# Optimization experiments

Measured on AMD Instinct MI355X. Metric: run time of the kernel, lower is better.

The kernel has to match this reference:

```python
import jax, jax.numpy as jnp
import numpy as np
import math

B, S, E, H = 2, 2048, 1024, 16
D = E // H  # head_dim = 64


def setup_inputs() -> dict:
    key = jax.random.key(0)
    ks = jax.random.split(key, 5)
    scale_p = 1.0 / math.sqrt(D)
    return {
        "x": jax.random.normal(ks[0], (B, S, E), dtype=jnp.float32),
        "Wq": jax.random.normal(ks[1], (D, D), dtype=jnp.float32) * scale_p,
        "Wk": jax.random.normal(ks[2], (D, D), dtype=jnp.float32) * scale_p,
        "Wv": jax.random.normal(ks[3], (D, D), dtype=jnp.float32) * scale_p,
        "W_out": jax.random.normal(ks[4], (E, E), dtype=jnp.float32) * (1.0 / math.sqrt(E)),
        "b_out": jnp.zeros((E,), dtype=jnp.float32),
    }


def reference(x, Wq, Wk, Wv, W_out, b_out):
    b, s, e = x.shape
    xh = x.reshape(b, s, H, D)  # [B,S,H,D]
    # per-head linear projections (torch Linear: y = x @ W.T), weights shared across heads
    q = jnp.einsum("bshd,ed->bshe", xh, Wq)
    k = jnp.einsum("bshd,ed->bshe", xh, Wk)
    v = jnp.einsum("bshd,ed->bshe", xh, Wv)
    # scaled dot-product attention, scale = sqrt(embed_dim) per tutorial-style impl
    energy = jnp.einsum("bqhd,bkhd->bhqk", q, k) / jnp.sqrt(jnp.float32(e))
    attn = jax.nn.softmax(energy, axis=-1)  # [B,H,S,S]
    out = jnp.einsum("bhqk,bkhd->bqhd", attn, v).reshape(b, s, e)
    return out @ W_out.T + b_out
```

## Files before the change

### kernel.cpp

```cpp
#include <hip/hip_runtime.h>
#include <math.h>

#define BB 2
#define SS 2048
#define EE 1024
#define HH 16
#define DD 64
constexpr int NROWS = BB * SS * HH;
constexpr float SCALE_Q = 1.4426950408889634f / 32.0f;

typedef __attribute__((ext_vector_type(8))) short bf16x8;
typedef __attribute__((ext_vector_type(4))) float f32x4;
typedef __attribute__((ext_vector_type(16))) float f32x16;
typedef __attribute__((ext_vector_type(4))) unsigned u32x4;

__device__ inline ushort f2bf(float f) {
  unsigned u = __builtin_bit_cast(unsigned, f);
  u += 0x7fffu + ((u >> 16) & 1u);
  return (ushort)(u >> 16);
}

__device__ inline unsigned cvt_pk(float lo, float hi) {
  unsigned r;
  asm("v_cvt_pk_bf16_f32 %0, %1, %2" : "=v"(r) : "v"(lo), "v"(hi));
  return r;
}

__global__ __launch_bounds__(256) void wconv(
    const float* __restrict__ Wq, const float* __restrict__ Wk,
    const float* __restrict__ Wv, const float* __restrict__ Wo,
    ushort* __restrict__ wqkvb, ushort* __restrict__ wob) {
  int idx = blockIdx.x * 256 + threadIdx.x;
  const float* sp;
  ushort* dp;
  if (idx < 1536) {
    int t = idx >> 9, j = idx & 511;
    const float* W = (t == 0) ? Wq : ((t == 1) ? Wk : Wv);
    sp = W + j * 8;
    dp = wqkvb + t * 4096 + j * 8;
  } else {
    size_t j = (size_t)(idx - 1536) * 8;
    sp = Wo + j;
    dp = wob + j;
  }
  float4 a = *(const float4*)sp;
  float4 c = *(const float4*)(sp + 4);
  u32x4 r;
  r[0] = cvt_pk(a.x, a.y);
  r[1] = cvt_pk(a.z, a.w);
  r[2] = cvt_pk(c.x, c.y);
  r[3] = cvt_pk(c.z, c.w);
  *(u32x4*)dp = r;
}

__global__ __launch_bounds__(256) void qkv_mfma(
    const float* __restrict__ x, const ushort* __restrict__ wqkv,
    ushort* __restrict__ qo, ushort* __restrict__ ko, ushort* __restrict__ vto) {
  __shared__ __align__(16) ushort Xs[128 * 72];
  __shared__ __align__(16) ushort Ws[3][64 * 72];
  const int tid = threadIdx.x, w = tid >> 6, l = tid & 63;
  const int g = l >> 4, c = l & 15;
  const int s0 = blockIdx.x * 128, h = blockIdx.y, b = blockIdx.z;

  for (int i = tid; i < 1536; i += 256) {
    int t = i >> 9, j = i & 511;
    int r = j >> 3, e0 = (j & 7) * 8;
    *(bf16x8*)&Ws[t][r * 72 + e0] = *(const bf16x8*)&wqkv[t * 4096 + r * 64 + e0];
  }
  for (int i = tid; i < 2048; i += 256) {
    int r = i >> 4, c4 = (i & 15) * 4;
    float4 xv = *(const float4*)&x[(((size_t)b * SS + s0 + r) * HH + h) * DD + c4];
    uint2 pk;
    pk.x = cvt_pk(xv.x, xv.y);
    pk.y = cvt_pk(xv.z, xv.w);
    *(uint2*)&Xs[r * 72 + c4] = pk;
  }
  __syncthreads();

  bf16x8 a_[2][2];
#pragma unroll
  for (int rf = 0; rf < 2; ++rf) {
    a_[rf][0] = *(bf16x8*)&Xs[(w * 32 + rf * 16 + c) * 72 + g * 8];
    a_[rf][1] = *(bf16x8*)&Xs[(w * 32 + rf * 16 + c) * 72 + 32 + g * 8];
  }

#pragma unroll
  for (int t = 0; t < 2; ++t) {
    ushort* out = (t == 0) ? qo : ko;
    const float sc = (t == 0) ? SCALE_Q : 1.0f;
#pragma unroll
    for (int ct = 0; ct < 4; ++ct) {
      bf16x8 b0 = *(bf16x8*)&Ws[t][(ct * 16 + c) * 72 + g * 8];
      bf16x8 b1 = *(bf16x8*)&Ws[t][(ct * 16 + c) * 72 + 32 + g * 8];
#pragma unroll
      for (int rf = 0; rf < 2; ++rf) {
        f32x4 acc = (f32x4){0.f, 0.f, 0.f, 0.f};
        acc = __builtin_amdgcn_mfma_f32_16x16x32_bf16(a_[rf][0], b0, acc, 0, 0, 0);
        acc = __builtin_amdgcn_mfma_f32_16x16x32_bf16(a_[rf][1], b1, acc, 0, 0, 0);
#pragma unroll
        for (int r = 0; r < 4; ++r) {
          int srow = w * 32 + rf * 16 + g * 4 + r;
          out[(((size_t)b * SS + s0 + srow) * HH + h) * DD + ct * 16 + c] =
              f2bf(acc[r] * sc);
        }
      }
    }
  }
#pragma unroll
  for (int ct = 0; ct < 4; ++ct) {
    bf16x8 b0 = *(bf16x8*)&Ws[2][(ct * 16 + c) * 72 + g * 8];
    bf16x8 b1 = *(bf16x8*)&Ws[2][(ct * 16 + c) * 72 + 32 + g * 8];
#pragma unroll
    for (int rf = 0; rf < 2; ++rf) {
      f32x4 acc = (f32x4){0.f, 0.f, 0.f, 0.f};
      acc = __builtin_amdgcn_mfma_f32_16x16x32_bf16(a_[rf][0], b0, acc, 0, 0, 0);
      acc = __builtin_amdgcn_mfma_f32_16x16x32_bf16(a_[rf][1], b1, acc, 0, 0, 0);
      uint2 pk;
      pk.x = cvt_pk(acc[0], acc[1]);
      pk.y = cvt_pk(acc[2], acc[3]);
      int d = ct * 16 + c;
      int srow = w * 32 + rf * 16 + g * 4;
      *(uint2*)&vto[(((size_t)b * HH + h) * DD + d) * SS + s0 + srow] = pk;
    }
  }
}

__global__ __launch_bounds__(256, 1) void attn_mfma(
    const ushort* __restrict__ q, const ushort* __restrict__ k,
    const ushort* __restrict__ vt, ushort* __restrict__ o) {
  __shared__ __align__(16) ushort Ks[2][64 * 72];
  __shared__ __align__(16) ushort Vts[2][64 * 72];
  const int tid = threadIdx.x, w = tid >> 6, l = tid & 63;
  const int lq = l & 31, h2 = l >> 5;
  const int work = ((blockIdx.x & 7) << 5) | (blockIdx.x >> 3);
  const int qt = work & 7, hb = work >> 3;
  const int h = hb & 15, b = hb >> 4;
  const int q0 = qt * 256 + w * 64;

  const size_t bh_qk = (size_t)b * SS * EE + h * DD;
  const size_t bh_vt = (size_t)b * SS * EE + h * (DD * SS);

  const int sr0 = tid >> 3;
  const int se0 = (tid & 7) * 8;
  const int krow0 = (sr0 & 19) | ((sr0 & 4) << 1) | ((sr0 & 8) >> 1);

  {
    bf16x8 kr0 = *(const bf16x8*)&k[bh_qk + (size_t)sr0 * EE + se0];
    bf16x8 kr1 = *(const bf16x8*)&k[bh_qk + (size_t)(sr0 + 32) * EE + se0];
    bf16x8 vr0 = *(const bf16x8*)&vt[bh_vt + (size_t)sr0 * SS + se0];
    bf16x8 vr1 = *(const bf16x8*)&vt[bh_vt + (size_t)(sr0 + 32) * SS + se0];
    *(bf16x8*)&Ks[0][krow0 * 72 + se0] = kr0;
    *(bf16x8*)&Ks[0][(krow0 + 32) * 72 + se0] = kr1;
    *(bf16x8*)&Vts[0][sr0 * 72 + se0] = vr0;
    *(bf16x8*)&Vts[0][(sr0 + 32) * 72 + se0] = vr1;
  }

  bf16x8 aq[2][4];
#pragma unroll
  for (int qb = 0; qb < 2; ++qb)
#pragma unroll
    for (int db = 0; db < 4; ++db)
      aq[qb][db] = *(const bf16x8*)&q[bh_qk +
          (size_t)(q0 + qb * 32 + lq) * EE + db * 16 + h2 * 8];

  f32x16 accO[2][2];
  float lacc[2][2];
#pragma unroll
  for (int qb = 0; qb < 2; ++qb) {
    lacc[qb][0] = 0.f;
    lacc[qb][1] = 0.f;
#pragma unroll
    for (int ct = 0; ct < 2; ++ct)
#pragma unroll
      for (int r = 0; r < 16; ++r) accO[qb][ct][r] = 0.f;
  }

  __syncthreads();

  for (int t = 0; t < 32; ++t) {
    const int cur = t & 1;
    bf16x8 kr0, kr1, vr0, vr1;
    if (t < 31) {
      const size_t kb2 = bh_qk + (size_t)((t + 1) * 64) * EE;
      kr0 = *(const bf16x8*)&k[kb2 + (size_t)sr0 * EE + se0];
      kr1 = *(const bf16x8*)&k[kb2 + (size_t)(sr0 + 32) * EE + se0];
      const size_t vb2 = bh_vt + (t + 1) * 64;
      vr0 = *(const bf16x8*)&vt[vb2 + (size_t)sr0 * SS + se0];
      vr1 = *(const bf16x8*)&vt[vb2 + (size_t)(sr0 + 32) * SS + se0];
    }

    bf16x8 kf[2][4];
#pragma unroll
    for (int kb = 0; kb < 2; ++kb)
#pragma unroll
      for (int db = 0; db < 4; ++db)
        kf[kb][db] = *(bf16x8*)&Ks[cur][(kb * 32 + lq) * 72 + db * 16 + h2 * 8];

    u32x4 pwv[2][2][2];
#pragma unroll
    for (int qb = 0; qb < 2; ++qb) {
      f32x16 s[2];
      __builtin_amdgcn_s_setprio(1);
#pragma unroll
      for (int kb = 0; kb < 2; ++kb) {
        f32x16 acc;
#pragma unroll
        for (int r = 0; r < 16; ++r) acc[r] = 0.f;
#pragma unroll
        for (int db = 0; db < 4; ++db)
          acc = __builtin_amdgcn_mfma_f32_32x32x16_bf16(kf[kb][db], aq[qb][db],
                                                        acc, 0, 0, 0);
        s[kb] = acc;
      }
      __builtin_amdgcn_s_setprio(0);
#pragma unroll
      for (int kb = 0; kb < 2; ++kb)
#pragma unroll
        for (int t16 = 0; t16 < 2; ++t16)
#pragma unroll
          for (int j2 = 0; j2 < 4; ++j2) {
            float pa = __builtin_amdgcn_exp2f(s[kb][t16 * 8 + j2 * 2]);
            float pb = __builtin_amdgcn_exp2f(s[kb][t16 * 8 + j2 * 2 + 1]);
            lacc[qb][kb] += pa + pb;
            pwv[qb][kb][t16][j2] = cvt_pk(pa, pb);
          }
    }

    bf16x8 vf[2][4];
#pragma unroll
    for (int ct = 0; ct < 2; ++ct)
#pragma unroll
      for (int kb = 0; kb < 2; ++kb)
#pragma unroll
        for (int t16 = 0; t16 < 2; ++t16)
          vf[ct][kb * 2 + t16] = *(bf16x8*)&Vts[cur][(ct * 32 + lq) * 72 +
                                                     kb * 32 + t16 * 16 + h2 * 8];

    __builtin_amdgcn_s_setprio(1);
#pragma unroll
    for (int ct = 0; ct < 2; ++ct)
#pragma unroll
      for (int kb = 0; kb < 2; ++kb)
#pragma unroll
        for (int t16 = 0; t16 < 2; ++t16) {
          accO[0][ct] = __builtin_amdgcn_mfma_f32_32x32x16_bf16(
              vf[ct][kb * 2 + t16],
              __builtin_bit_cast(bf16x8, pwv[0][kb][t16]), accO[0][ct], 0, 0, 0);
          accO[1][ct] = __builtin_amdgcn_mfma_f32_32x32x16_bf16(
              vf[ct][kb * 2 + t16],
              __builtin_bit_cast(bf16x8, pwv[1][kb][t16]), accO[1][ct], 0, 0, 0);
        }
    __builtin_amdgcn_s_setprio(0);

    if (t < 31) {
      const int nxt = cur ^ 1;
      *(bf16x8*)&Ks[nxt][krow0 * 72 + se0] = kr0;
      *(bf16x8*)&Ks[nxt][(krow0 + 32) * 72 + se0] = kr1;
      *(bf16x8*)&Vts[nxt][sr0 * 72 + se0] = vr0;
      *(bf16x8*)&Vts[nxt][(sr0 + 32) * 72 + se0] = vr1;
    }
    __syncthreads();
  }

#pragma unroll
  for (int qb = 0; qb < 2; ++qb) {
    float tsum = lacc[qb][0] + lacc[qb][1];
    tsum += __shfl_xor(tsum, 32, 64);
    float inv = 1.f / tsum;
    size_t row = (size_t)b * SS + q0 + qb * 32 + lq;
#pragma unroll
    for (int ct = 0; ct < 2; ++ct)
#pragma unroll
      for (int rq = 0; rq < 4; ++rq) {
        uint2 pk;
        pk.x = cvt_pk(accO[qb][ct][rq * 4 + 0] * inv,
                      accO[qb][ct][rq * 4 + 1] * inv);
        pk.y = cvt_pk(accO[qb][ct][rq * 4 + 2] * inv,
                      accO[qb][ct][rq * 4 + 3] * inv);
        *(uint2*)&o[row * EE + h * DD + ct * 32 + rq * 8 + h2 * 4] = pk;
      }
  }
}

__global__ __launch_bounds__(256) void out_proj_mfma(
    const ushort* __restrict__ a, const ushort* __restrict__ wo,
    const float* __restrict__ bias, float* __restrict__ y) {
  __shared__ __align__(16) ushort As[2][128 * 72];
  __shared__ __align__(16) ushort Ws[2][64 * 72];
  const int tid = threadIdx.x, w = tid >> 6, l = tid & 63;
  const int g = l >> 4, c = l & 15;
  const int m0 = blockIdx.x * 128, n0 = blockIdx.y * 64;
  const int sr = tid >> 3, se = (tid & 7) * 8;

  f32x4 acc[2][4];
#pragma unroll
  for (int mf = 0; mf < 2; ++mf)
#pragma unroll
    for (int ct = 0; ct < 4; ++ct) acc[mf][ct] = (f32x4){0.f, 0.f, 0.f, 0.f};

  {
#pragma unroll
    for (int j = 0; j < 4; ++j) {
      int r = sr + j * 32;
      *(bf16x8*)&As[0][r * 72 + se] = *(const bf16x8*)&a[(size_t)(m0 + r) * EE + se];
    }
#pragma unroll
    for (int j = 0; j < 2; ++j) {
      int r = sr + j * 32;
      *(bf16x8*)&Ws[0][r * 72 + se] = *(const bf16x8*)&wo[(size_t)(n0 + r) * EE + se];
    }
  }
  __syncthreads();

  for (int t = 0; t < 16; ++t) {
    const int cur = t & 1;
    bf16x8 Arg[4], Brg[2];
    if (t < 15) {
      const int k0 = (t + 1) * 64;
#pragma unroll
      for (int j = 0; j < 4; ++j) {
        int r = sr + j * 32;
        Arg[j] = *(const bf16x8*)&a[(size_t)(m0 + r) * EE + k0 + se];
      }
#pragma unroll
      for (int j = 0; j < 2; ++j) {
        int r = sr + j * 32;
        Brg[j] = *(const bf16x8*)&wo[(size_t)(n0 + r) * EE + k0 + se];
      }
    }

    bf16x8 af[2][2];
#pragma unroll
    for (int mf = 0; mf < 2; ++mf) {
      af[mf][0] = *(bf16x8*)&As[cur][(w * 32 + mf * 16 + c) * 72 + g * 8];
      af[mf][1] = *(bf16x8*)&As[cur][(w * 32 + mf * 16 + c) * 72 + 32 + g * 8];
    }
    __builtin_amdgcn_s_setprio(1);
#pragma unroll
    for (int ct = 0; ct < 4; ++ct) {
      bf16x8 b0 = *(bf16x8*)&Ws[cur][(ct * 16 + c) * 72 + g * 8];
      bf16x8 b1 = *(bf16x8*)&Ws[cur][(ct * 16 + c) * 72 + 32 + g * 8];
#pragma unroll
      for (int mf = 0; mf < 2; ++mf) {
        acc[mf][ct] = __builtin_amdgcn_mfma_f32_16x16x32_bf16(af[mf][0], b0, acc[mf][ct], 0, 0, 0);
        acc[mf][ct] = __builtin_amdgcn_mfma_f32_16x16x32_bf16(af[mf][1], b1, acc[mf][ct], 0, 0, 0);
      }
    }
    __builtin_amdgcn_s_setprio(0);

    if (t < 15) {
      const int nxt = cur ^ 1;
#pragma unroll
      for (int j = 0; j < 4; ++j) {
        int r = sr + j * 32;
        *(bf16x8*)&As[nxt][r * 72 + se] = Arg[j];
      }
#pragma unroll
      for (int j = 0; j < 2; ++j) {
        int r = sr + j * 32;
        *(bf16x8*)&Ws[nxt][r * 72 + se] = Brg[j];
      }
    }
    __syncthreads();
  }

#pragma unroll
  for (int ct = 0; ct < 4; ++ct) {
    float bv = bias[n0 + ct * 16 + c];
#pragma unroll
    for (int mf = 0; mf < 2; ++mf)
#pragma unroll
      for (int r = 0; r < 4; ++r)
        y[(size_t)(m0 + w * 32 + mf * 16 + g * 4 + r) * EE + n0 + ct * 16 + c] =
            acc[mf][ct][r] + bv;
  }
}

extern "C" void kernel_launch(void* const* d_in, const int* in_sizes, int n_in,
                              void* d_out, int out_size, void* d_ws,
                              size_t ws_size, hipStream_t stream) {
  const float* x = (const float*)d_in[0];
  const float* Wq = (const float*)d_in[1];
  const float* Wk = (const float*)d_in[2];
  const float* Wv = (const float*)d_in[3];
  const float* Wo = (const float*)d_in[4];
  const float* bo = (const float*)d_in[5];
  float* out = (float*)d_out;

  const size_t per = (size_t)NROWS * 64;
  ushort* qb = (ushort*)d_ws;
  ushort* kb = qb + per;
  ushort* vtb = kb + per;
  ushort* aob = vtb + per;
  ushort* wob = aob + per;
  ushort* wqkvb = wob + 1024 * 1024;

  wconv<<<518, 256, 0, stream>>>(Wq, Wk, Wv, Wo, wqkvb, wob);
  qkv_mfma<<<dim3(16, 16, 2), 256, 0, stream>>>(x, wqkvb, qb, kb, vtb);
  attn_mfma<<<256, 256, 0, stream>>>(qb, kb, vtb, aob);
  out_proj_mfma<<<dim3(32, 16), 256, 0, stream>>>(aob, wob, bo, out);
}
```

Baseline: 87.44 us.

## Halve per-wave query rows, double attention grid, software-pipeline PV with next QK

Each wave now handles 32 query rows instead of 64, so the attention grid doubles to 512 blocks and the launch bound no longer pins one block per CU, which lowers register pressure and raises occupancy. The loop is software-pipelined: the PV MFMA for the previous tile's probabilities runs alongside the current tile's QK^T and exp, with a prologue and epilogue added. K/V tiles are now loaded twice as often per query row, increasing global/LDS traffic, and the setprio hints are removed.

```diff
diff --git a/kernel.cpp b/kernel.cpp
--- a/kernel.cpp
+++ b/kernel.cpp
@@ -125,17 +125,17 @@
   }
 }
 
-__global__ __launch_bounds__(256, 1) void attn_mfma(
+__global__ __launch_bounds__(256) void attn_mfma(
     const ushort* __restrict__ q, const ushort* __restrict__ k,
     const ushort* __restrict__ vt, ushort* __restrict__ o) {
   __shared__ __align__(16) ushort Ks[2][64 * 72];
   __shared__ __align__(16) ushort Vts[2][64 * 72];
   const int tid = threadIdx.x, w = tid >> 6, l = tid & 63;
   const int lq = l & 31, h2 = l >> 5;
-  const int work = ((blockIdx.x & 7) << 5) | (blockIdx.x >> 3);
-  const int qt = work & 7, hb = work >> 3;
+  const int work = ((blockIdx.x & 7) << 6) | (blockIdx.x >> 3);
+  const int qt = work & 15, hb = work >> 4;
   const int h = hb & 15, b = hb >> 4;
-  const int q0 = qt * 256 + w * 64;
+  const int q0 = qt * 128 + w * 32;
 
   const size_t bh_qk = (size_t)b * SS * EE + h * DD;
   const size_t bh_vt = (size_t)b * SS * EE + h * (DD * SS);
@@ -155,104 +155,129 @@
     *(bf16x8*)&Vts[0][(sr0 + 32) * 72 + se0] = vr1;
   }
 
-  bf16x8 aq[2][4];
-#pragma unroll
-  for (int qb = 0; qb < 2; ++qb)
-#pragma unroll
-    for (int db = 0; db < 4; ++db)
-      aq[qb][db] = *(const bf16x8*)&q[bh_qk +
-          (size_t)(q0 + qb * 32 + lq) * EE + db * 16 + h2 * 8];
-
-  f32x16 accO[2][2];
-  float lacc[2][2];
-#pragma unroll
-  for (int qb = 0; qb < 2; ++qb) {
-    lacc[qb][0] = 0.f;
-    lacc[qb][1] = 0.f;
+  bf16x8 aq[4];
+#pragma unroll
+  for (int db = 0; db < 4; ++db)
+    aq[db] = *(const bf16x8*)&q[bh_qk + (size_t)(q0 + lq) * EE + db * 16 + h2 * 8];
+
+  f32x16 accO[2];
+  float lacc[2] = {0.f, 0.f};
+#pragma unroll
+  for (int ct = 0; ct < 2; ++ct)
+#pragma unroll
+    for (int r = 0; r < 16; ++r) accO[ct][r] = 0.f;
+
+  u32x4 pwvP[2][2];
+  bf16x8 vfP[2][4];
+
+  __syncthreads();
+
+  {
+    bf16x8 kr0 = *(const bf16x8*)&k[bh_qk + (size_t)(64 + sr0) * EE + se0];
+    bf16x8 kr1 = *(const bf16x8*)&k[bh_qk + (size_t)(64 + sr0 + 32) * EE + se0];
+    bf16x8 vr0 = *(const bf16x8*)&vt[bh_vt + 64 + (size_t)sr0 * SS + se0];
+    bf16x8 vr1 = *(const bf16x8*)&vt[bh_vt + 64 + (size_t)(sr0 + 32) * SS + se0];
+
+    f32x16 s[2];
+#pragma unroll
+    for (int kb = 0; kb < 2; ++kb) {
+      f32x16 acc;
+#pragma unroll
+      for (int r = 0; r < 16; ++r) acc[r] = 0.f;
+#pragma unroll
+      for (int db = 0; db < 4; ++db) {
+        bf16x8 ka = *(bf16x8*)&Ks[0][(kb * 32 + lq) * 72 + db * 16 + h2 * 8];
+        acc = __builtin_amdgcn_mfma_f32_32x32x16_bf16(ka, aq[db], acc, 0, 0, 0);
+      }
+      s[kb] = acc;
+    }
+#pragma unroll
+    for (int kb = 0; kb < 2; ++kb)
+#pragma unroll
+      for (int t16 = 0; t16 < 2; ++t16)
+#pragma unroll
+        for (int j2 = 0; j2 < 4; ++j2) {
+          float pa = __builtin_amdgcn_exp2f(s[kb][t16 * 8 + j2 * 2]);
+          float pb = __builtin_amdgcn_exp2f(s[kb][t16 * 8 + j2 * 2 + 1]);
+          lacc[kb] += pa + pb;
+          pwvP[kb][t16][j2] = cvt_pk(pa, pb);
+        }
 #pragma unroll
     for (int ct = 0; ct < 2; ++ct)
 #pragma unroll
-      for (int r = 0; r < 16; ++r) accO[qb][ct][r] = 0.f;
-  }
-
-  __syncthreads();
-
-  for (int t = 0; t < 32; ++t) {
+      for (int kb = 0; kb < 2; ++kb)
+#pragma unroll
+        for (int t16 = 0; t16 < 2; ++t16)
+          vfP[ct][kb * 2 + t16] = *(bf16x8*)&Vts[0][(ct * 32 + lq) * 72 +
+                                                    kb * 32 + t16 * 16 + h2 * 8];
+    *(bf16x8*)&Ks[1][krow0 * 72 + se0] = kr0;
+    *(bf16x8*)&Ks[1][(krow0 + 32) * 72 + se0] = kr1;
+    *(bf16x8*)&Vts[1][sr0 * 72 + se0] = vr0;
+    *(bf16x8*)&Vts[1][(sr0 + 32) * 72 + se0] = vr1;
+    __syncthreads();
+  }
+
+  for (int t = 1; t < 32; ++t) {
     const int cur = t & 1;
+    const int tn = (t + 1) & 31;
+
     bf16x8 kr0, kr1, vr0, vr1;
-    if (t < 31) {
-      const size_t kb2 = bh_qk + (size_t)((t + 1) * 64) * EE;
+    {
+      const size_t kb2 = bh_qk + (size_t)(tn * 64) * EE;
       kr0 = *(const bf16x8*)&k[kb2 + (size_t)sr0 * EE + se0];
       kr1 = *(const bf16x8*)&k[kb2 + (size_t)(sr0 + 32) * EE + se0];
-      const size_t vb2 = bh_vt + (t + 1) * 64;
+      const size_t vb2 = bh_vt + tn * 64;
       vr0 = *(const bf16x8*)&vt[vb2 + (size_t)sr0 * SS + se0];
       vr1 = *(const bf16x8*)&vt[vb2 + (size_t)(sr0 + 32) * SS + se0];
     }
 
-    bf16x8 kf[2][4];
+    f32x16 s[2];
+#pragma unroll
+    for (int kb = 0; kb < 2; ++kb) {
+      f32x16 acc;
+#pragma unroll
+      for (int r = 0; r < 16; ++r) acc[r] = 0.f;
+#pragma unroll
+      for (int db = 0; db < 4; ++db) {
+        bf16x8 ka = *(bf16x8*)&Ks[cur][(kb * 32 + lq) * 72 + db * 16 + h2 * 8];
+        acc = __builtin_amdgcn_mfma_f32_32x32x16_bf16(ka, aq[db], acc, 0, 0, 0);
+      }
+      s[kb] = acc;
+    }
+
+#pragma unroll
+    for (int ct = 0; ct < 2; ++ct)
+#pragma unroll
+      for (int kb = 0; kb < 2; ++kb)
+#pragma unroll
+        for (int t16 = 0; t16 < 2; ++t16)
+          accO[ct] = __builtin_amdgcn_mfma_f32_32x32x16_bf16(
+              vfP[ct][kb * 2 + t16],
+              __builtin_bit_cast(bf16x8, pwvP[kb][t16]), accO[ct], 0, 0, 0);
+
+    u32x4 pwvC[2][2];
 #pragma unroll
     for (int kb = 0; kb < 2; ++kb)
 #pragma unroll
-      for (int db = 0; db < 4; ++db)
-        kf[kb][db] = *(bf16x8*)&Ks[cur][(kb * 32 + lq) * 72 + db * 16 + h2 * 8];
-
-    u32x4 pwv[2][2][2];
-#pragma unroll
-    for (int qb = 0; qb < 2; ++qb) {
-      f32x16 s[2];
-      __builtin_amdgcn_s_setprio(1);
-#pragma unroll
-      for (int kb = 0; kb < 2; ++kb) {
-        f32x16 acc;
-#pragma unroll
-        for (int r = 0; r < 16; ++r) acc[r] = 0.f;
-#pragma unroll
-        for (int db = 0; db < 4; ++db)
-          acc = __builtin_amdgcn_mfma_f32_32x32x16_bf16(kf[kb][db], aq[qb][db],
-                                                        acc, 0, 0, 0);
-        s[kb] = acc;
-      }
-      __builtin_amdgcn_s_setprio(0);
+      for (int t16 = 0; t16 < 2; ++t16)
+#pragma unroll
+        for (int j2 = 0; j2 < 4; ++j2) {
+          float pa = __builtin_amdgcn_exp2f(s[kb][t16 * 8 + j2 * 2]);
+          float pb = __builtin_amdgcn_exp2f(s[kb][t16 * 8 + j2 * 2 + 1]);
+          lacc[kb] += pa + pb;
+          pwvC[kb][t16][j2] = cvt_pk(pa, pb);
+        }
+
+#pragma unroll
+    for (int ct = 0; ct < 2; ++ct)
 #pragma unroll
       for (int kb = 0; kb < 2; ++kb)
 #pragma unroll
         for (int t16 = 0; t16 < 2; ++t16)
-#pragma unroll
-          for (int j2 = 0; j2 < 4; ++j2) {
-            float pa = __builtin_amdgcn_exp2f(s[kb][t16 * 8 + j2 * 2]);
-            float pb = __builtin_amdgcn_exp2f(s[kb][t16 * 8 + j2 * 2 + 1]);
-            lacc[qb][kb] += pa + pb;
-            pwv[qb][kb][t16][j2] = cvt_pk(pa, pb);
-          }
-    }
-
-    bf16x8 vf[2][4];
-#pragma unroll
-    for (int ct = 0; ct < 2; ++ct)
-#pragma unroll
-      for (int kb = 0; kb < 2; ++kb)
-#pragma unroll
-        for (int t16 = 0; t16 < 2; ++t16)
-          vf[ct][kb * 2 + t16] = *(bf16x8*)&Vts[cur][(ct * 32 + lq) * 72 +
-                                                     kb * 32 + t16 * 16 + h2 * 8];
-
-    __builtin_amdgcn_s_setprio(1);
-#pragma unroll
-    for (int ct = 0; ct < 2; ++ct)
-#pragma unroll
-      for (int kb = 0; kb < 2; ++kb)
-#pragma unroll
-        for (int t16 = 0; t16 < 2; ++t16) {
-          accO[0][ct] = __builtin_amdgcn_mfma_f32_32x32x16_bf16(
-              vf[ct][kb * 2 + t16],
-              __builtin_bit_cast(bf16x8, pwv[0][kb][t16]), accO[0][ct], 0, 0, 0);
-          accO[1][ct] = __builtin_amdgcn_mfma_f32_32x32x16_bf16(
-              vf[ct][kb * 2 + t16],
-              __builtin_bit_cast(bf16x8, pwv[1][kb][t16]), accO[1][ct], 0, 0, 0);
-        }
-    __builtin_amdgcn_s_setprio(0);
-
-    if (t < 31) {
+          vfP[ct][kb * 2 + t16] = *(bf16x8*)&Vts[cur][(ct * 32 + lq) * 72 +
+                                                      kb * 32 + t16 * 16 + h2 * 8];
+
+    {
       const int nxt = cur ^ 1;
       *(bf16x8*)&Ks[nxt][krow0 * 72 + se0] = kr0;
       *(bf16x8*)&Ks[nxt][(krow0 + 32) * 72 + se0] = kr1;
@@ -260,23 +285,35 @@
       *(bf16x8*)&Vts[nxt][(sr0 + 32) * 72 + se0] = vr1;
     }
     __syncthreads();
-  }
-
-#pragma unroll
-  for (int qb = 0; qb < 2; ++qb) {
-    float tsum = lacc[qb][0] + lacc[qb][1];
+
+#pragma unroll
+    for (int kb = 0; kb < 2; ++kb)
+#pragma unroll
+      for (int t16 = 0; t16 < 2; ++t16) pwvP[kb][t16] = pwvC[kb][t16];
+  }
+
+#pragma unroll
+  for (int ct = 0; ct < 2; ++ct)
+#pragma unroll
+    for (int kb = 0; kb < 2; ++kb)
+#pragma unroll
+      for (int t16 = 0; t16 < 2; ++t16)
+        accO[ct] = __builtin_amdgcn_mfma_f32_32x32x16_bf16(
+            vfP[ct][kb * 2 + t16],
+            __builtin_bit_cast(bf16x8, pwvP[kb][t16]), accO[ct], 0, 0, 0);
+
+  {
+    float tsum = lacc[0] + lacc[1];
     tsum += __shfl_xor(tsum, 32, 64);
     float inv = 1.f / tsum;
-    size_t row = (size_t)b * SS + q0 + qb * 32 + lq;
+    size_t row = (size_t)b * SS + q0 + lq;
 #pragma unroll
     for (int ct = 0; ct < 2; ++ct)
 #pragma unroll
       for (int rq = 0; rq < 4; ++rq) {
         uint2 pk;
-        pk.x = cvt_pk(accO[qb][ct][rq * 4 + 0] * inv,
-                      accO[qb][ct][rq * 4 + 1] * inv);
-        pk.y = cvt_pk(accO[qb][ct][rq * 4 + 2] * inv,
-                      accO[qb][ct][rq * 4 + 3] * inv);
+        pk.x = cvt_pk(accO[ct][rq * 4 + 0] * inv, accO[ct][rq * 4 + 1] * inv);
+        pk.y = cvt_pk(accO[ct][rq * 4 + 2] * inv, accO[ct][rq * 4 + 3] * inv);
         *(uint2*)&o[row * EE + h * DD + ct * 32 + rq * 8 + h2 * 4] = pk;
       }
   }
@@ -397,6 +434,6 @@
 
   wconv<<<518, 256, 0, stream>>>(Wq, Wk, Wv, Wo, wqkvb, wob);
   qkv_mfma<<<dim3(16, 16, 2), 256, 0, stream>>>(x, wqkvb, qb, kb, vtb);
-  attn_mfma<<<256, 256, 0, stream>>>(qb, kb, vtb, aob);
+  attn_mfma<<<512, 256, 0, stream>>>(qb, kb, vtb, aob);
   out_proj_mfma<<<dim3(32, 16), 256, 0, stream>>>(aob, wob, bo, out);
 }
```

New measurement: 81.51 us. 1.07x faster.
